# Optimization experiments

Measured on AMD Instinct MI355X. Metric: run time of the kernel, lower is better.

## Reference

```python
import jax, jax.numpy as jnp
import numpy as np

D = 256          # d_model
NH = 8           # heads
NP = 4           # points per level
NL = 4           # feature levels
DH = D // NH     # head dim = 32
MLP = 4 * D      # 1024
B = 2
SHAPES = [(128, 128), (64, 64), (32, 32), (16, 16)]
LQ = sum(h * w for h, w in SHAPES)  # 21760
EPS = 1e-6


def layer_norm(x, g, b):
    mu = jnp.mean(x, axis=-1, keepdims=True)
    var = jnp.mean(jnp.square(x - mu), axis=-1, keepdims=True)
    return (x - mu) * jax.lax.rsqrt(var + EPS) * g + b


def bilinear_sample(val_l, loc, Hs, Ws):
    # val_l: [B, Hs*Ws, NH, DH]; loc: [B, Lq, NH, NP, 2] normalized in [0,1]
    v = val_l.transpose(0, 2, 1, 3)                      # [B, NH, HW, DH]
    x = loc[..., 0] * Ws - 0.5                           # [B, Lq, NH, NP]
    y = loc[..., 1] * Hs - 0.5
    x0 = jnp.floor(x); y0 = jnp.floor(y)
    lx = x - x0; ly = y - y0
    x0i = x0.astype(jnp.int32); y0i = y0.astype(jnp.int32)

    def gather(xi, yi):
        inb = (xi >= 0) & (xi < Ws) & (yi >= 0) & (yi < Hs)
        idx = jnp.clip(yi, 0, Hs - 1) * Ws + jnp.clip(xi, 0, Ws - 1)
        idx = idx.transpose(0, 2, 1, 3)                  # [B, NH, Lq, NP]
        sh = idx.shape
        idxf = idx.reshape(sh[0], sh[1], -1)
        g = jax.vmap(jax.vmap(lambda vv, ii: vv[ii]))(v, idxf)
        g = g.reshape(sh[0], sh[1], sh[2], sh[3], v.shape[-1])
        return g * inb.transpose(0, 2, 1, 3)[..., None].astype(g.dtype)

    wt = lambda a: a.transpose(0, 2, 1, 3)[..., None]    # -> [B, NH, Lq, NP, 1]
    out = (gather(x0i, y0i) * wt((1 - lx) * (1 - ly))
           + gather(x0i + 1, y0i) * wt(lx * (1 - ly))
           + gather(x0i, y0i + 1) * wt((1 - lx) * ly)
           + gather(x0i + 1, y0i + 1) * wt(lx * ly))
    return out                                            # [B, NH, Lq, NP, DH]


def setup_inputs() -> dict:
    key = jax.random.key(0)
    ks = jax.random.split(key, 16)
    ss = np.array(SHAPES, dtype=np.int64)
    lsi = np.concatenate([[0], np.cumsum(ss[:, 0] * ss[:, 1])[:-1]]).astype(np.int64)
    s = 0.02
    return {
        'src': jax.random.normal(ks[0], (B, LQ, D), jnp.float32),
        'pos': jax.random.normal(ks[1], (B, LQ, D), jnp.float32),
        'reference_points': jax.random.uniform(ks[2], (B, LQ, NL, 2), jnp.float32),
        'spatial_shapes': ss,
        'level_start_index': lsi,
        'g1': jnp.ones((D,), jnp.float32), 'beta1': jnp.zeros((D,), jnp.float32),
        'w_off': jax.random.normal(ks[3], (D, NH * NL * NP * 2), jnp.float32) * 0.01,
        'b_off': jax.random.normal(ks[4], (NH * NL * NP * 2,), jnp.float32) * 0.1,
        'w_attn': jax.random.normal(ks[5], (D, NH * NL * NP), jnp.float32) * s,
        'b_attn': jnp.zeros((NH * NL * NP,), jnp.float32),
        'w_val': jax.random.normal(ks[6], (D, D), jnp.float32) * s,
        'b_val': jnp.zeros((D,), jnp.float32),
        'w_out': jax.random.normal(ks[7], (D, D), jnp.float32) * s,
        'b_out': jnp.zeros((D,), jnp.float32),
        'g2': jnp.ones((D,), jnp.float32), 'beta2': jnp.zeros((D,), jnp.float32),
        'w_fc1': jax.random.normal(ks[8], (D, MLP), jnp.float32) * s,
        'b_fc1': jnp.zeros((MLP,), jnp.float32),
        'w_fc2': jax.random.normal(ks[9], (MLP, D), jnp.float32) * s,
        'b_fc2': jnp.zeros((D,), jnp.float32),
    }


def reference(src, pos, reference_points, spatial_shapes, level_start_index,
              g1, beta1, w_off, b_off, w_attn, b_attn, w_val, b_val,
              w_out, b_out, g2, beta2, w_fc1, b_fc1, w_fc2, b_fc2):
    ss = np.asarray(spatial_shapes)
    lsi = np.asarray(level_start_index)
    Bsz, Lq, _ = src.shape

    # --- pre-norm + multi-scale deformable attention + residual ---
    x = layer_norm(src, g1, beta1)
    q = x + pos
    val = (x @ w_val + b_val).reshape(Bsz, Lq, NH, DH)
    off = (q @ w_off + b_off).reshape(Bsz, Lq, NH, NL, NP, 2)
    aw = jax.nn.softmax((q @ w_attn + b_attn).reshape(Bsz, Lq, NH, NL * NP), axis=-1)
    aw = aw.reshape(Bsz, Lq, NH, NL, NP)

    out = jnp.zeros((Bsz, Lq, NH, DH), src.dtype)
    for l in range(NL):
        Hs, Ws = int(ss[l, 0]), int(ss[l, 1])
        start = int(lsi[l])
        vl = val[:, start:start + Hs * Ws]                       # [B, HW, NH, DH]
        norm = jnp.array([Ws, Hs], src.dtype)
        loc = reference_points[:, :, None, l, None, :] + off[:, :, :, l] / norm
        samp = bilinear_sample(vl, loc, Hs, Ws)                  # [B, NH, Lq, NP, DH]
        a = aw[:, :, :, l].transpose(0, 2, 1, 3)                 # [B, NH, Lq, NP]
        out = out + jnp.einsum('bhqp,bhqpd->bqhd', a, samp)
    attn_out = out.reshape(Bsz, Lq, D) @ w_out + b_out
    src2 = src + attn_out

    # --- pre-norm MLP + residual ---
    y = layer_norm(src2, g2, beta2)
    ffn = jax.nn.relu(y @ w_fc1 + b_fc1) @ w_fc2 + b_fc2
    return src2 + ffn
```

## Files before the change

### kernel.cpp

```cpp
#include <hip/hip_runtime.h>

#define DMODEL 256
#define NHEAD 8
#define NPOINT 4
#define NLEVEL 4
#define DHEAD 32
#define MLPD 1024
#define BSZ 2
#define LQTOK 21760
#define NTOK (BSZ * LQTOK)
#define LNEPS 1e-6f

typedef __attribute__((ext_vector_type(8))) short short8;
typedef __attribute__((ext_vector_type(4))) float f32x4;
typedef __attribute__((ext_vector_type(2))) float f32x2;

__device__ __forceinline__ float bf2f(unsigned short u) {
  unsigned int i = ((unsigned int)u) << 16;
  return __builtin_bit_cast(float, i);
}
__device__ __forceinline__ unsigned short f2bf(float f) {
  unsigned int i = __builtin_bit_cast(unsigned int, f);
  i += 0x7fff + ((i >> 16) & 1);
  return (unsigned short)(i >> 16);
}
__device__ __forceinline__ float bflo(unsigned int u) {
  return __builtin_bit_cast(float, u << 16);
}
__device__ __forceinline__ float bfhi(unsigned int u) {
  return __builtin_bit_cast(float, u & 0xffff0000u);
}

__device__ __forceinline__ void pk_fma_blo(f32x2& d, f32x2 a, f32x2 b) {
  asm("v_pk_fma_f32 %0, %1, %2, %0 op_sel:[0,0,0] op_sel_hi:[1,0,1]"
      : "+v"(d)
      : "v"(a), "v"(b));
}
__device__ __forceinline__ void pk_fma_bhi(f32x2& d, f32x2 a, f32x2 b) {
  asm("v_pk_fma_f32 %0, %1, %2, %0 op_sel:[0,1,0] op_sel_hi:[1,1,1]"
      : "+v"(d)
      : "v"(a), "v"(b));
}

__device__ __forceinline__ void gload_lds16(const unsigned short* g,
                                            unsigned short* lds) {
  __builtin_amdgcn_global_load_lds(
      (const __attribute__((address_space(1))) unsigned int*)g,
      (__attribute__((address_space(3))) unsigned int*)lds, 16, 0, 0);
}

__device__ __forceinline__ unsigned xcd_swz(unsigned orig, unsigned nwg) {
  unsigned xcd = orig & 7u, rest = orig >> 3;
  unsigned qq = nwg >> 3, rr = nwg & 7u;
  return (xcd < rr ? xcd * (qq + 1) : rr * (qq + 1) + (xcd - rr) * qq) + rest;
}

template <bool EMITQ>
__global__ __launch_bounds__(256) void ln_bf16(
    const float* __restrict__ in, const float* __restrict__ g,
    const float* __restrict__ beta, unsigned short* __restrict__ o,
    const float* __restrict__ pos, unsigned short* __restrict__ q) {
  const int w = threadIdx.x >> 6, lane = threadIdx.x & 63;
  const size_t t = (size_t)blockIdx.x * 4 + w;
  const size_t base = t * DMODEL + lane * 4;
  float4 v = *(const float4*)(in + base);
  float s = (v.x + v.y) + (v.z + v.w);
#pragma unroll
  for (int off = 32; off; off >>= 1) s += __shfl_xor(s, off, 64);
  float mu = s * (1.0f / DMODEL);
  float dx = v.x - mu, dy = v.y - mu, dz = v.z - mu, dw = v.w - mu;
  float s2 = (dx * dx + dy * dy) + (dz * dz + dw * dw);
#pragma unroll
  for (int off = 32; off; off >>= 1) s2 += __shfl_xor(s2, off, 64);
  float rs = rsqrtf(s2 * (1.0f / DMODEL) + LNEPS);
  float4 gg = *(const float4*)(g + lane * 4);
  float4 bb = *(const float4*)(beta + lane * 4);
  unsigned short r0 = f2bf(dx * rs * gg.x + bb.x);
  unsigned short r1 = f2bf(dy * rs * gg.y + bb.y);
  unsigned short r2 = f2bf(dz * rs * gg.z + bb.z);
  unsigned short r3 = f2bf(dw * rs * gg.w + bb.w);
  unsigned int lo = ((unsigned int)r1 << 16) | r0;
  unsigned int hi = ((unsigned int)r3 << 16) | r2;
  *(uint2*)(o + base) = make_uint2(lo, hi);
  if (EMITQ) {
    float4 p = *(const float4*)(pos + base);
    unsigned short q0 = f2bf(bf2f(r0) + p.x);
    unsigned short q1 = f2bf(bf2f(r1) + p.y);
    unsigned short q2 = f2bf(bf2f(r2) + p.z);
    unsigned short q3 = f2bf(bf2f(r3) + p.w);
    unsigned int ql = ((unsigned int)q1 << 16) | q0;
    unsigned int qh = ((unsigned int)q3 << 16) | q2;
    *(uint2*)(q + base) = make_uint2(ql, qh);
  }
}

__global__ __launch_bounds__(256) void transpose_all(
    const float* __restrict__ w_val, const float* __restrict__ w_off,
    const float* __restrict__ w_attn, const float* __restrict__ w_out,
    const float* __restrict__ w_fc1, const float* __restrict__ w_fc2,
    unsigned short* __restrict__ wvalT, unsigned short* __restrict__ woffaT,
    unsigned short* __restrict__ woutT, unsigned short* __restrict__ wfc1T,
    unsigned short* __restrict__ wfc2T) {
  __shared__ float tile[32][33];
  int bid = blockIdx.x;
  const float* W;
  unsigned short* Wt;
  int K, N, rel;
  if (bid < 64) {
    W = w_val; Wt = wvalT; K = 256; N = 256; rel = bid;
  } else if (bid < 128) {
    W = w_off; Wt = woffaT; K = 256; N = 256; rel = bid - 64;
  } else if (bid < 160) {
    W = w_attn; Wt = woffaT + 256 * 256; K = 256; N = 128; rel = bid - 128;
  } else if (bid < 224) {
    W = w_out; Wt = woutT; K = 256; N = 256; rel = bid - 160;
  } else if (bid < 480) {
    W = w_fc1; Wt = wfc1T; K = 256; N = 1024; rel = bid - 224;
  } else {
    W = w_fc2; Wt = wfc2T; K = 1024; N = 256; rel = bid - 480;
  }
  int ktiles = K >> 5;
  int k0 = (rel % ktiles) * 32, n0 = (rel / ktiles) * 32;
  int tx = threadIdx.x & 31, ty = threadIdx.x >> 5;
  for (int i = ty; i < 32; i += 8)
    tile[i][tx] = W[(size_t)(k0 + i) * N + n0 + tx];
  __syncthreads();
  for (int i = ty; i < 32; i += 8)
    Wt[(size_t)(n0 + i) * K + k0 + tx] = f2bf(tile[tx][i]);
}

template <int OMODE>
__global__ __launch_bounds__(256) void gemm_mfma(
    const unsigned short* __restrict__ A, const unsigned short* __restrict__ Wt,
    const float* __restrict__ bias, const float* __restrict__ res,
    void* __restrict__ Cout, int M, int N, int K) {
  __shared__ __attribute__((aligned(16))) unsigned short As[128 * 32];
  __shared__ __attribute__((aligned(16))) unsigned short Bs[128 * 32];
  const int tid = threadIdx.x;
  const unsigned gy = gridDim.y;
  const unsigned wgid = xcd_swz(blockIdx.y * gridDim.x + blockIdx.x,
                                gridDim.x * gy);
  const int m0 = (int)(wgid / gy) * 128;
  const int n0 = (int)(wgid % gy) * 128;
  const int wave = tid >> 6, lane = tid & 63;
  const int wm = (wave & 1) * 64, wn = (wave >> 1) * 64;
  const int lr = lane & 15, quad = lane >> 4;
  f32x4 acc[4][4] = {};
  for (int k0 = 0; k0 < K; k0 += 32) {
    __syncthreads();
#pragma unroll
    for (int r = 0; r < 2; r++) {
      int c = r * 256 + tid;
      int row = c >> 2, col8 = (c & 3) * 8;
      gload_lds16(Wt + (size_t)(n0 + row) * K + k0 + col8,
                  &Bs[(r * 256 + wave * 64) * 8]);
    }
#pragma unroll
    for (int r = 0; r < 2; r++) {
      int c = r * 256 + tid;
      int row = c >> 2, col8 = (c & 3) * 8;
      gload_lds16(A + (size_t)(m0 + row) * K + k0 + col8,
                  &As[(r * 256 + wave * 64) * 8]);
    }
    __syncthreads();
    short8 af[4], bfr[4];
#pragma unroll
    for (int i = 0; i < 4; i++)
      af[i] = *(const short8*)(&As[(wm + i * 16 + lr) * 32 + quad * 8]);
#pragma unroll
    for (int j = 0; j < 4; j++)
      bfr[j] = *(const short8*)(&Bs[(wn + j * 16 + lr) * 32 + quad * 8]);
#pragma unroll
    for (int i = 0; i < 4; i++)
#pragma unroll
      for (int j = 0; j < 4; j++)
        acc[i][j] = __builtin_amdgcn_mfma_f32_16x16x32_bf16(af[i], bfr[j],
                                                            acc[i][j], 0, 0, 0);
  }
#pragma unroll
  for (int i = 0; i < 4; i++) {
    int rbase = m0 + wm + i * 16 + quad * 4;
#pragma unroll
    for (int j = 0; j < 4; j++) {
      int col = n0 + wn + j * 16 + lr;
      float bv = bias[col];
#pragma unroll
      for (int r = 0; r < 4; r++) {
        size_t idx = (size_t)(rbase + r) * N + col;
        float v = acc[i][j][r] + bv;
        if (OMODE == 2) v = fmaxf(v, 0.0f);
        if (OMODE == 3) {
          ((float*)Cout)[idx] = v + res[idx];
        } else {
          ((unsigned short*)Cout)[idx] = f2bf(v);
        }
      }
    }
  }
}

__global__ __launch_bounds__(256) void gemm_vo(
    const unsigned short* __restrict__ Ax, const unsigned short* __restrict__ Aq,
    const unsigned short* __restrict__ Wval,
    const unsigned short* __restrict__ Woa, const float* __restrict__ bval,
    const float* __restrict__ boff, const float* __restrict__ battn,
    unsigned short* __restrict__ oval, unsigned short* __restrict__ ooff,
    unsigned short* __restrict__ olg) {
  __shared__ __attribute__((aligned(16))) unsigned short As[128 * 32];
  __shared__ __attribute__((aligned(16))) unsigned short Bs[128 * 32];
  const int tid = threadIdx.x;
  const unsigned gy = gridDim.y;
  const unsigned wgid = xcd_swz(blockIdx.y * gridDim.x + blockIdx.x,
                                gridDim.x * gy);
  const int m0 = (int)(wgid / gy) * 128;
  const int ny = (int)(wgid % gy);
  const bool isval = ny < 2;
  const unsigned short* A = isval ? Ax : Aq;
  const unsigned short* Wt = isval ? Wval : Woa;
  const int n0 = isval ? ny * 128 : (ny - 2) * 128;
  const int wave = tid >> 6, lane = tid & 63;
  const int wm = (wave & 1) * 64, wn = (wave >> 1) * 64;
  const int lr = lane & 15, quad = lane >> 4;
  f32x4 acc[4][4] = {};
  for (int k0 = 0; k0 < 256; k0 += 32) {
    __syncthreads();
#pragma unroll
    for (int r = 0; r < 2; r++) {
      int c = r * 256 + tid;
      int row = c >> 2, col8 = (c & 3) * 8;
      gload_lds16(Wt + (size_t)(n0 + row) * 256 + k0 + col8,
                  &Bs[(r * 256 + wave * 64) * 8]);
    }
#pragma unroll
    for (int r = 0; r < 2; r++) {
      int c = r * 256 + tid;
      int row = c >> 2, col8 = (c & 3) * 8;
      gload_lds16(A + (size_t)(m0 + row) * 256 + k0 + col8,
                  &As[(r * 256 + wave * 64) * 8]);
    }
    __syncthreads();
    short8 af[4], bfr[4];
#pragma unroll
    for (int i = 0; i < 4; i++)
      af[i] = *(const short8*)(&As[(wm + i * 16 + lr) * 32 + quad * 8]);
#pragma unroll
    for (int j = 0; j < 4; j++)
      bfr[j] = *(const short8*)(&Bs[(wn + j * 16 + lr) * 32 + quad * 8]);
#pragma unroll
    for (int i = 0; i < 4; i++)
#pragma unroll
      for (int j = 0; j < 4; j++)
        acc[i][j] = __builtin_amdgcn_mfma_f32_16x16x32_bf16(af[i], bfr[j],
                                                            acc[i][j], 0, 0, 0);
  }
#pragma unroll
  for (int i = 0; i < 4; i++) {
    int rbase = m0 + wm + i * 16 + quad * 4;
#pragma unroll
    for (int j = 0; j < 4; j++) {
      int col = n0 + wn + j * 16 + lr;
      float bv = isval ? bval[col]
                       : (col < 256 ? boff[col] : battn[col - 256]);
#pragma unroll
      for (int r = 0; r < 4; r++) {
        size_t row = (size_t)(rbase + r);
        float v = acc[i][j][r] + bv;
        if (isval) {
          oval[row * 256 + col] = f2bf(v);
        } else if (col < 256) {
          ooff[row * 256 + col] = f2bf(v);
        } else {
          olg[row * 128 + (col - 256)] = f2bf(v);
        }
      }
    }
  }
}

__global__ __launch_bounds__(512) void deform_sample(
    const unsigned short* __restrict__ val, const unsigned short* __restrict__ off,
    const unsigned short* __restrict__ logits, const float* __restrict__ refp,
    unsigned short* __restrict__ out) {
  __shared__ __attribute__((aligned(16))) int sIdx[8][16][8][4];
  __shared__ __attribute__((aligned(16))) float sW[8][16][8][4];
  const int w = threadIdx.x >> 6, lane = threadIdx.x & 63;
  const int bq = blockIdx.x * 8 + w;
  const int b = __builtin_amdgcn_readfirstlane(bq / LQTOK);
  {
    const int HW_[4] = {128, 64, 32, 16};
    const int LSI_[4] = {0, 16384, 20480, 21504};
    int u0 = 2 * lane;
    int h = u0 >> 4;
    int lvl = (u0 >> 2) & 3;
    int pt0 = u0 & 15;
    int HW = HW_[lvl];
    float2 rp = ((const float2*)refp)[(size_t)bq * 4 + lvl];
    uint2 ov = *(const uint2*)(off + (size_t)bq * 256 + 4 * lane);
    unsigned int lgu = *(const unsigned int*)(logits + (size_t)bq * 128 + 2 * lane);
    float lg0 = bflo(lgu), lg1 = bfhi(lgu);
    float mx = fmaxf(lg0, lg1);
#pragma unroll
    for (int s = 1; s < 8; s <<= 1) mx = fmaxf(mx, __shfl_xor(mx, s, 64));
    float e0 = expf(lg0 - mx), e1 = expf(lg1 - mx);
    float es = e0 + e1;
#pragma unroll
    for (int s = 1; s < 8; s <<= 1) es += __shfl_xor(es, s, 64);
    float inv = 1.0f / es;
    float a01[2] = {e0 * inv, e1 * inv};
    unsigned int ovv[2] = {ov.x, ov.y};
    int hb2 = h * (DHEAD * 2);
#pragma unroll
    for (int c = 0; c < 2; c++) {
      float x = fmaf(rp.x, (float)HW, bflo(ovv[c])) - 0.5f;
      float y = fmaf(rp.y, (float)HW, bfhi(ovv[c])) - 0.5f;
      float xf = floorf(x), yf = floorf(y);
      int x0 = (int)xf, y0 = (int)yf;
      float lx = x - xf, ly = y - yf;
      int x0c = min(max(x0, 0), HW - 1);
      int x1c = min(max(x0 + 1, 0), HW - 1);
      int y0c = min(max(y0, 0), HW - 1);
      int y1c = min(max(y0 + 1, 0), HW - 1);
      float m0x = (x0 >= 0 && x0 < HW) ? 1.f : 0.f;
      float m1x = (x0 + 1 >= 0 && x0 + 1 < HW) ? 1.f : 0.f;
      float m0y = (y0 >= 0 && y0 < HW) ? 1.f : 0.f;
      float m1y = (y0 + 1 >= 0 && y0 + 1 < HW) ? 1.f : 0.f;
      float a = a01[c];
      int pt = pt0 + c;
      int hs = h ^ (pt & 7);
      int r0 = (LSI_[lvl] + y0c * HW) * (DMODEL * 2) + hb2;
      int r1 = (LSI_[lvl] + y1c * HW) * (DMODEL * 2) + hb2;
      *(int4*)sIdx[w][pt][hs] =
          make_int4(r0 + x0c * (DMODEL * 2), r0 + x1c * (DMODEL * 2),
                    r1 + x0c * (DMODEL * 2), r1 + x1c * (DMODEL * 2));
      *(float4*)sW[w][pt][hs] =
          make_float4((1.f - lx) * (1.f - ly) * m0x * m0y * a,
                      lx * (1.f - ly) * m1x * m0y * a,
                      (1.f - lx) * ly * m0x * m1y * a,
                      lx * ly * m1x * m1y * a);
    }
  }
  __builtin_amdgcn_wave_barrier();
  const int h2 = lane >> 3, g = lane & 7;
  const char* basep =
      (const char*)val + (size_t)b * ((size_t)LQTOK * DMODEL * 2);
  const int goff = g * 8;
  f32x2 a01v = {0.f, 0.f}, a23v = {0.f, 0.f};
#pragma unroll
  for (int pb = 0; pb < 4; pb++) {
    int4 ix[4];
    f32x4 wt4[4];
#pragma unroll
    for (int p = 0; p < 4; p++) {
      int pt = pb * 4 + p;
      int hs = h2 ^ (pt & 7);
      ix[p] = *(const int4*)sIdx[w][pt][hs];
      wt4[p] = *(const f32x4*)sW[w][pt][hs];
    }
    uint2 v4[4][4];
#pragma unroll
    for (int p = 0; p < 4; p++) {
      v4[p][0] = *(const uint2*)(basep + (unsigned)(ix[p].x + goff));
      v4[p][1] = *(const uint2*)(basep + (unsigned)(ix[p].y + goff));
      v4[p][2] = *(const uint2*)(basep + (unsigned)(ix[p].z + goff));
      v4[p][3] = *(const uint2*)(basep + (unsigned)(ix[p].w + goff));
    }
#pragma unroll
    for (int p = 0; p < 4; p++) {
      f32x2 w01 = __builtin_shufflevector(wt4[p], wt4[p], 0, 1);
      f32x2 w23 = __builtin_shufflevector(wt4[p], wt4[p], 2, 3);
#pragma unroll
      for (int k = 0; k < 4; k++) {
        uint2 u = v4[p][k];
        f32x2 vlo, vhi;
        vlo[0] = bflo(u.x);
        vlo[1] = bfhi(u.x);
        vhi[0] = bflo(u.y);
        vhi[1] = bfhi(u.y);
        f32x2 wp = (k < 2) ? w01 : w23;
        if ((k & 1) == 0) {
          pk_fma_blo(a01v, vlo, wp);
          pk_fma_blo(a23v, vhi, wp);
        } else {
          pk_fma_bhi(a01v, vlo, wp);
          pk_fma_bhi(a23v, vhi, wp);
        }
      }
    }
  }
  unsigned int o0 = ((unsigned int)f2bf(a01v[1]) << 16) | f2bf(a01v[0]);
  unsigned int o1 = ((unsigned int)f2bf(a23v[1]) << 16) | f2bf(a23v[0]);
  *(uint2*)(out + (size_t)bq * 256 + h2 * 32 + g * 4) = make_uint2(o0, o1);
}

extern "C" void kernel_launch(void* const* d_in, const int* in_sizes, int n_in,
                              void* d_out, int out_size, void* d_ws,
                              size_t ws_size, hipStream_t stream) {
  const float* src    = (const float*)d_in[0];
  const float* pos    = (const float*)d_in[1];
  const float* refp   = (const float*)d_in[2];
  const float* g1     = (const float*)d_in[5];
  const float* beta1  = (const float*)d_in[6];
  const float* w_off  = (const float*)d_in[7];
  const float* b_off  = (const float*)d_in[8];
  const float* w_attn = (const float*)d_in[9];
  const float* b_attn = (const float*)d_in[10];
  const float* w_val  = (const float*)d_in[11];
  const float* b_val  = (const float*)d_in[12];
  const float* w_out  = (const float*)d_in[13];
  const float* b_out  = (const float*)d_in[14];
  const float* g2     = (const float*)d_in[15];
  const float* beta2  = (const float*)d_in[16];
  const float* w_fc1  = (const float*)d_in[17];
  const float* b_fc1  = (const float*)d_in[18];
  const float* w_fc2  = (const float*)d_in[19];
  const float* b_fc2  = (const float*)d_in[20];
  float* out = (float*)d_out;

  const size_t NT = (size_t)NTOK;
  unsigned short* b1 = (unsigned short*)d_ws;
  unsigned short* b2 = b1 + NT * 256;
  unsigned short* b3 = b2 + NT * 256;
  unsigned short* b4 = b3 + NT * 256;
  unsigned short* b5 = b4 + NT * 256;
  unsigned short* wvalT  = b5 + NT * 512;
  unsigned short* woffaT = wvalT + 256 * 256;
  unsigned short* woutT  = woffaT + 384 * 256;
  unsigned short* wfc1T  = woutT + 256 * 256;
  unsigned short* wfc2T  = wfc1T + 1024 * 256;

  unsigned short* qb  = b4;
  unsigned short* lgb = b5;
  unsigned short* yb  = b5;
  unsigned short* hid = b1;

  const int MT = NTOK / 128;

  transpose_all<<<736, 256, 0, stream>>>(w_val, w_off, w_attn, w_out, w_fc1,
                                         w_fc2, wvalT, woffaT, woutT, wfc1T,
                                         wfc2T);
  ln_bf16<true><<<NTOK / 4, 256, 0, stream>>>(src, g1, beta1, b1, pos, qb);
  gemm_vo<<<dim3(MT, 5), 256, 0, stream>>>(b1, qb, wvalT, woffaT, b_val, b_off,
                                           b_attn, b2, b3, lgb);
  deform_sample<<<NTOK / 8, 512, 0, stream>>>(b2, b3, lgb, refp, b1);
  gemm_mfma<3><<<dim3(MT, 2), 256, 0, stream>>>(b1, woutT, b_out, src, out,
                                                NTOK, 256, 256);
  ln_bf16<false><<<NTOK / 4, 256, 0, stream>>>(out, g2, beta2, yb, nullptr,
                                               nullptr);
  gemm_mfma<2><<<dim3(MT, 8), 256, 0, stream>>>(yb, wfc1T, b_fc1, nullptr, hid,
                                                NTOK, 1024, 256);
  gemm_mfma<3><<<dim3(MT, 2), 256, 0, stream>>>(hid, wfc2T, b_fc2, out, out,
                                                NTOK, 256, 1024);
}
```

Measured before the change: 415.0 us.

## Fuse out-projection with LayerNorm2 and use head-major value layout in sampling

Adds a gemm_out_ln kernel that computes the output projection with a full-row 64x256 tile, adds bias and residual, and applies the second LayerNorm in the epilogue. This removes the separate LN pass and its extra read of src2. The value projection now writes a head-major [B,NH,Lq,32] layout, and the bilinear sampler loads two adjacent x pixels as one 16-byte load per row. Each wave splits its lanes across the pair and combines them with a shuffle, cutting the number of gather instructions. The fused LN uses single-pass E[x^2]-mu^2 variance, which is less numerically robust, and a border clamp trick is needed to handle x at the edges.

```diff
diff --git a/kernel.cpp b/kernel.cpp
--- a/kernel.cpp
+++ b/kernel.cpp
@@ -55,7 +55,6 @@
   return (xcd < rr ? xcd * (qq + 1) : rr * (qq + 1) + (xcd - rr) * qq) + rest;
 }
 
-template <bool EMITQ>
 __global__ __launch_bounds__(256) void ln_bf16(
     const float* __restrict__ in, const float* __restrict__ g,
     const float* __restrict__ beta, unsigned short* __restrict__ o,
@@ -82,16 +81,14 @@
   unsigned int lo = ((unsigned int)r1 << 16) | r0;
   unsigned int hi = ((unsigned int)r3 << 16) | r2;
   *(uint2*)(o + base) = make_uint2(lo, hi);
-  if (EMITQ) {
-    float4 p = *(const float4*)(pos + base);
-    unsigned short q0 = f2bf(bf2f(r0) + p.x);
-    unsigned short q1 = f2bf(bf2f(r1) + p.y);
-    unsigned short q2 = f2bf(bf2f(r2) + p.z);
-    unsigned short q3 = f2bf(bf2f(r3) + p.w);
-    unsigned int ql = ((unsigned int)q1 << 16) | q0;
-    unsigned int qh = ((unsigned int)q3 << 16) | q2;
-    *(uint2*)(q + base) = make_uint2(ql, qh);
-  }
+  float4 p = *(const float4*)(pos + base);
+  unsigned short q0 = f2bf(bf2f(r0) + p.x);
+  unsigned short q1 = f2bf(bf2f(r1) + p.y);
+  unsigned short q2 = f2bf(bf2f(r2) + p.z);
+  unsigned short q3 = f2bf(bf2f(r3) + p.w);
+  unsigned int ql = ((unsigned int)q1 << 16) | q0;
+  unsigned int qh = ((unsigned int)q3 << 16) | q2;
+  *(uint2*)(q + base) = make_uint2(ql, qh);
 }
 
 __global__ __launch_bounds__(256) void transpose_all(
@@ -263,25 +260,129 @@
                        : (col < 256 ? boff[col] : battn[col - 256]);
 #pragma unroll
       for (int r = 0; r < 4; r++) {
-        size_t row = (size_t)(rbase + r);
+        int row = rbase + r;
         float v = acc[i][j][r] + bv;
         if (isval) {
-          oval[row * 256 + col] = f2bf(v);
+          int b_ = row >= LQTOK ? 1 : 0;
+          int lq = row - b_ * LQTOK;
+          int h = col >> 5, cc = col & 31;
+          oval[(((size_t)b_ * 8 + h) * LQTOK + lq) * 32 + cc] = f2bf(v);
         } else if (col < 256) {
-          ooff[row * 256 + col] = f2bf(v);
+          ooff[(size_t)row * 256 + col] = f2bf(v);
         } else {
-          olg[row * 128 + (col - 256)] = f2bf(v);
+          olg[(size_t)row * 128 + (col - 256)] = f2bf(v);
         }
       }
     }
   }
+}
+
+__global__ __launch_bounds__(256) void gemm_out_ln(
+    const unsigned short* __restrict__ A, const unsigned short* __restrict__ Wt,
+    const float* __restrict__ bias, const float* __restrict__ src,
+    const float* __restrict__ g2, const float* __restrict__ beta2,
+    float* __restrict__ src2, unsigned short* __restrict__ y) {
+  __shared__ __attribute__((aligned(16))) unsigned short As[64 * 32];
+  __shared__ __attribute__((aligned(16))) unsigned short Bs[256 * 32];
+  __shared__ float red[2][64][2];
+  const int tid = threadIdx.x;
+  const int m0 = (int)blockIdx.x * 64;
+  const int wave = tid >> 6, lane = tid & 63;
+  const int wm = (wave >> 1) * 32, wn = (wave & 1) * 128;
+  const int lr = lane & 15, quad = lane >> 4;
+  f32x4 acc[2][8] = {};
+  for (int k0 = 0; k0 < 256; k0 += 32) {
+    __syncthreads();
+    {
+      int row = tid >> 2, col8 = (tid & 3) * 8;
+      gload_lds16(A + (size_t)(m0 + row) * 256 + k0 + col8,
+                  &As[(wave * 64) * 8]);
+    }
+#pragma unroll
+    for (int r = 0; r < 4; r++) {
+      int c = r * 256 + tid;
+      int row = c >> 2, col8 = (c & 3) * 8;
+      gload_lds16(Wt + (size_t)row * 256 + k0 + col8,
+                  &Bs[(r * 256 + wave * 64) * 8]);
+    }
+    __syncthreads();
+    short8 af[2], bfr[8];
+#pragma unroll
+    for (int i = 0; i < 2; i++)
+      af[i] = *(const short8*)(&As[(wm + i * 16 + lr) * 32 + quad * 8]);
+#pragma unroll
+    for (int j = 0; j < 8; j++)
+      bfr[j] = *(const short8*)(&Bs[(wn + j * 16 + lr) * 32 + quad * 8]);
+#pragma unroll
+    for (int i = 0; i < 2; i++)
+#pragma unroll
+      for (int j = 0; j < 8; j++)
+        acc[i][j] = __builtin_amdgcn_mfma_f32_16x16x32_bf16(af[i], bfr[j],
+                                                            acc[i][j], 0, 0, 0);
+  }
+  float s1[2][4] = {}, s2[2][4] = {};
+#pragma unroll
+  for (int i = 0; i < 2; i++)
+#pragma unroll
+    for (int j = 0; j < 8; j++) {
+      int col = wn + j * 16 + lr;
+      float bv = bias[col];
+#pragma unroll
+      for (int r = 0; r < 4; r++) {
+        int row = m0 + wm + i * 16 + quad * 4 + r;
+        size_t idx = (size_t)row * 256 + col;
+        float v = acc[i][j][r] + bv + src[idx];
+        src2[idx] = v;
+        acc[i][j][r] = v;
+        s1[i][r] += v;
+        s2[i][r] = fmaf(v, v, s2[i][r]);
+      }
+    }
+#pragma unroll
+  for (int i = 0; i < 2; i++)
+#pragma unroll
+    for (int r = 0; r < 4; r++)
+#pragma unroll
+      for (int s = 1; s < 16; s <<= 1) {
+        s1[i][r] += __shfl_xor(s1[i][r], s, 64);
+        s2[i][r] += __shfl_xor(s2[i][r], s, 64);
+      }
+  if (lr == 0) {
+#pragma unroll
+    for (int i = 0; i < 2; i++)
+#pragma unroll
+      for (int r = 0; r < 4; r++) {
+        int rl = wm + i * 16 + quad * 4 + r;
+        red[0][rl][wave & 1] = s1[i][r];
+        red[1][rl][wave & 1] = s2[i][r];
+      }
+  }
+  __syncthreads();
+#pragma unroll
+  for (int i = 0; i < 2; i++)
+#pragma unroll
+    for (int r = 0; r < 4; r++) {
+      int rl = wm + i * 16 + quad * 4 + r;
+      float S1 = red[0][rl][0] + red[0][rl][1];
+      float S2 = red[1][rl][0] + red[1][rl][1];
+      float mu = S1 * (1.0f / DMODEL);
+      float var = S2 * (1.0f / DMODEL) - mu * mu;
+      float rs = rsqrtf(var + LNEPS);
+      int row = m0 + rl;
+#pragma unroll
+      for (int j = 0; j < 8; j++) {
+        int col = wn + j * 16 + lr;
+        float yv = (acc[i][j][r] - mu) * rs * g2[col] + beta2[col];
+        y[(size_t)row * 256 + col] = f2bf(yv);
+      }
+    }
 }
 
 __global__ __launch_bounds__(512) void deform_sample(
     const unsigned short* __restrict__ val, const unsigned short* __restrict__ off,
     const unsigned short* __restrict__ logits, const float* __restrict__ refp,
     unsigned short* __restrict__ out) {
-  __shared__ __attribute__((aligned(16))) int sIdx[8][16][8][4];
+  __shared__ __attribute__((aligned(16))) int2 sIdx[8][16][8];
   __shared__ __attribute__((aligned(16))) float sW[8][16][8][4];
   const int w = threadIdx.x >> 6, lane = threadIdx.x & 63;
   const int bq = blockIdx.x * 8 + w;
@@ -308,7 +409,6 @@
     float inv = 1.0f / es;
     float a01[2] = {e0 * inv, e1 * inv};
     unsigned int ovv[2] = {ov.x, ov.y};
-    int hb2 = h * (DHEAD * 2);
 #pragma unroll
     for (int c = 0; c < 2; c++) {
       float x = fmaf(rp.x, (float)HW, bflo(ovv[c])) - 0.5f;
@@ -325,71 +425,74 @@
       float m0y = (y0 >= 0 && y0 < HW) ? 1.f : 0.f;
       float m1y = (y0 + 1 >= 0 && y0 + 1 < HW) ? 1.f : 0.f;
       float a = a01[c];
+      float w00 = (1.f - lx) * (1.f - ly) * m0x * m0y * a;
+      float w01 = lx * (1.f - ly) * m1x * m0y * a;
+      float w10 = (1.f - lx) * ly * m0x * m1y * a;
+      float w11 = lx * ly * m1x * m1y * a;
+      int xb = min(max(x0, 0), HW - 2);
+      bool c0 = (x0c == xb), c1 = (x1c == xb);
+      float A0 = (c0 ? w00 : 0.f) + (c1 ? w01 : 0.f);
+      float B0 = (c0 ? 0.f : w00) + (c1 ? 0.f : w01);
+      float A1 = (c0 ? w10 : 0.f) + (c1 ? w11 : 0.f);
+      float B1 = (c0 ? 0.f : w10) + (c1 ? 0.f : w11);
       int pt = pt0 + c;
       int hs = h ^ (pt & 7);
-      int r0 = (LSI_[lvl] + y0c * HW) * (DMODEL * 2) + hb2;
-      int r1 = (LSI_[lvl] + y1c * HW) * (DMODEL * 2) + hb2;
-      *(int4*)sIdx[w][pt][hs] =
-          make_int4(r0 + x0c * (DMODEL * 2), r0 + x1c * (DMODEL * 2),
-                    r1 + x0c * (DMODEL * 2), r1 + x1c * (DMODEL * 2));
-      *(float4*)sW[w][pt][hs] =
-          make_float4((1.f - lx) * (1.f - ly) * m0x * m0y * a,
-                      lx * (1.f - ly) * m1x * m0y * a,
-                      (1.f - lx) * ly * m0x * m1y * a,
-                      lx * ly * m1x * m1y * a);
+      sIdx[w][pt][hs] = make_int2((LSI_[lvl] + y0c * HW + xb) * 64,
+                                  (LSI_[lvl] + y1c * HW + xb) * 64);
+      *(float4*)sW[w][pt][hs] = make_float4(A0, B0, A1, B1);
     }
   }
   __builtin_amdgcn_wave_barrier();
   const int h2 = lane >> 3, g = lane & 7;
-  const char* basep =
-      (const char*)val + (size_t)b * ((size_t)LQTOK * DMODEL * 2);
-  const int goff = g * 8;
-  f32x2 a01v = {0.f, 0.f}, a23v = {0.f, 0.f};
+  const char* base2 = (const char*)val +
+                      ((size_t)(b * 8 + h2) * LQTOK) * 64 + g * 16;
+  f32x2 a4[4] = {};
 #pragma unroll
   for (int pb = 0; pb < 4; pb++) {
-    int4 ix[4];
+    int2 tt[4];
     f32x4 wt4[4];
 #pragma unroll
     for (int p = 0; p < 4; p++) {
       int pt = pb * 4 + p;
       int hs = h2 ^ (pt & 7);
-      ix[p] = *(const int4*)sIdx[w][pt][hs];
+      tt[p] = sIdx[w][pt][hs];
       wt4[p] = *(const f32x4*)sW[w][pt][hs];
     }
-    uint2 v4[4][4];
+    uint4 v0[4], v1[4];
 #pragma unroll
     for (int p = 0; p < 4; p++) {
-      v4[p][0] = *(const uint2*)(basep + (unsigned)(ix[p].x + goff));
-      v4[p][1] = *(const uint2*)(basep + (unsigned)(ix[p].y + goff));
-      v4[p][2] = *(const uint2*)(basep + (unsigned)(ix[p].z + goff));
-      v4[p][3] = *(const uint2*)(basep + (unsigned)(ix[p].w + goff));
+      v0[p] = *(const uint4*)(base2 + (unsigned)tt[p].x);
+      v1[p] = *(const uint4*)(base2 + (unsigned)tt[p].y);
     }
 #pragma unroll
     for (int p = 0; p < 4; p++) {
-      f32x2 w01 = __builtin_shufflevector(wt4[p], wt4[p], 0, 1);
-      f32x2 w23 = __builtin_shufflevector(wt4[p], wt4[p], 2, 3);
-#pragma unroll
-      for (int k = 0; k < 4; k++) {
-        uint2 u = v4[p][k];
-        f32x2 vlo, vhi;
-        vlo[0] = bflo(u.x);
-        vlo[1] = bfhi(u.x);
-        vhi[0] = bflo(u.y);
-        vhi[1] = bfhi(u.y);
-        f32x2 wp = (k < 2) ? w01 : w23;
-        if ((k & 1) == 0) {
-          pk_fma_blo(a01v, vlo, wp);
-          pk_fma_blo(a23v, vhi, wp);
-        } else {
-          pk_fma_bhi(a01v, vlo, wp);
-          pk_fma_bhi(a23v, vhi, wp);
-        }
-      }
-    }
-  }
-  unsigned int o0 = ((unsigned int)f2bf(a01v[1]) << 16) | f2bf(a01v[0]);
-  unsigned int o1 = ((unsigned int)f2bf(a23v[1]) << 16) | f2bf(a23v[0]);
-  *(uint2*)(out + (size_t)bq * 256 + h2 * 32 + g * 4) = make_uint2(o0, o1);
+      f32x2 wp;
+      wp[0] = (g < 4) ? wt4[p][0] : wt4[p][1];
+      wp[1] = (g < 4) ? wt4[p][2] : wt4[p][3];
+      f32x2 u;
+      u[0] = bflo(v0[p].x); u[1] = bfhi(v0[p].x); pk_fma_blo(a4[0], u, wp);
+      u[0] = bflo(v0[p].y); u[1] = bfhi(v0[p].y); pk_fma_blo(a4[1], u, wp);
+      u[0] = bflo(v0[p].z); u[1] = bfhi(v0[p].z); pk_fma_blo(a4[2], u, wp);
+      u[0] = bflo(v0[p].w); u[1] = bfhi(v0[p].w); pk_fma_blo(a4[3], u, wp);
+      u[0] = bflo(v1[p].x); u[1] = bfhi(v1[p].x); pk_fma_bhi(a4[0], u, wp);
+      u[0] = bflo(v1[p].y); u[1] = bfhi(v1[p].y); pk_fma_bhi(a4[1], u, wp);
+      u[0] = bflo(v1[p].z); u[1] = bfhi(v1[p].z); pk_fma_bhi(a4[2], u, wp);
+      u[0] = bflo(v1[p].w); u[1] = bfhi(v1[p].w); pk_fma_bhi(a4[3], u, wp);
+    }
+  }
+#pragma unroll
+  for (int qv = 0; qv < 4; qv++) {
+    a4[qv][0] += __shfl_xor(a4[qv][0], 4, 64);
+    a4[qv][1] += __shfl_xor(a4[qv][1], 4, 64);
+  }
+  if (g < 4) {
+    uint4 o;
+    o.x = ((unsigned)f2bf(a4[0][1]) << 16) | f2bf(a4[0][0]);
+    o.y = ((unsigned)f2bf(a4[1][1]) << 16) | f2bf(a4[1][0]);
+    o.z = ((unsigned)f2bf(a4[2][1]) << 16) | f2bf(a4[2][0]);
+    o.w = ((unsigned)f2bf(a4[3][1]) << 16) | f2bf(a4[3][0]);
+    *(uint4*)(out + (size_t)bq * 256 + h2 * 32 + g * 8) = o;
+  }
 }
 
 extern "C" void kernel_launch(void* const* d_in, const int* in_sizes, int n_in,
@@ -438,14 +541,12 @@
   transpose_all<<<736, 256, 0, stream>>>(w_val, w_off, w_attn, w_out, w_fc1,
                                          w_fc2, wvalT, woffaT, woutT, wfc1T,
                                          wfc2T);
-  ln_bf16<true><<<NTOK / 4, 256, 0, stream>>>(src, g1, beta1, b1, pos, qb);
+  ln_bf16<<<NTOK / 4, 256, 0, stream>>>(src, g1, beta1, b1, pos, qb);
   gemm_vo<<<dim3(MT, 5), 256, 0, stream>>>(b1, qb, wvalT, woffaT, b_val, b_off,
                                            b_attn, b2, b3, lgb);
   deform_sample<<<NTOK / 8, 512, 0, stream>>>(b2, b3, lgb, refp, b1);
-  gemm_mfma<3><<<dim3(MT, 2), 256, 0, stream>>>(b1, woutT, b_out, src, out,
-                                                NTOK, 256, 256);
-  ln_bf16<false><<<NTOK / 4, 256, 0, stream>>>(out, g2, beta2, yb, nullptr,
-                                               nullptr);
+  gemm_out_ln<<<NTOK / 64, 256, 0, stream>>>(b1, woutT, b_out, src, g2, beta2,
+                                             out, yb);
   gemm_mfma<2><<<dim3(MT, 8), 256, 0, stream>>>(yb, wfc1T, b_fc1, nullptr, hid,
                                                 NTOK, 1024, 256);
   gemm_mfma<3><<<dim3(MT, 2), 256, 0, stream>>>(hid, wfc2T, b_fc2, out, out,
```

Measured after the change: 412.4 us. Within noise of the previous version (-0.6%).
